# Optimization experiments

Measured on AMD Instinct MI355X. Metric: run time of the kernel, lower is better.

The kernel has to match this reference:

```python
import jax, jax.numpy as jnp
import numpy as np

N, D, H, C, E = 16384, 768, 768, 2, 20

def setup_inputs() -> dict:
    key = jax.random.key(0)
    k1, k2, k3, k4, k5, k6 = jax.random.split(key, 6)
    return {
        "embeddings": jax.random.normal(k1, (N, D), dtype=jnp.float32),
        "component_idx": jax.random.randint(k2, (N,), 0, E, dtype=jnp.int64),
        "W1": jax.random.normal(k3, (E, D, H), dtype=jnp.float32) * (1.0 / np.sqrt(D)),
        "b1": jnp.zeros((E, H), dtype=jnp.float32),
        "W2": jax.random.normal(k4, (E, H, C), dtype=jnp.float32) * (1.0 / np.sqrt(H)),
        "b2": jnp.zeros((E, C), dtype=jnp.float32),
    }

def reference(embeddings, component_idx, W1, b1, W2, b2):
    # Each token n goes through expert component_idx[n]:
    #   y = relu(x @ W1[e] + b1[e]) @ W2[e] + b2[e]
    # The torch module's mask/cat/argsort reassembly is mathematically a
    # per-token select of its own expert's output at the original position.
    # Dense-expert formulation (standard jax MoE fallback), then gather.
    h = jax.nn.relu(jnp.einsum('nd,edh->enh', embeddings, W1) + b1[:, None, :])  # [E,N,H]
    y = jnp.einsum('enh,ehc->enc', h, W2) + b2[:, None, :]                        # [E,N,C]
    n_idx = jnp.arange(embeddings.shape[0])
    return y[component_idx, n_idx]  # [N,C]
```

## Files before the change

kernel.cpp:

```cpp
#include <hip/hip_runtime.h>

#define N_D 768
#define N_H 768
#define N_C 2
#define N_E 20
#define MT 128
#define NT 128
#define BK 32
#define KT (N_D / BK)
#define MAX_TILES 160
#define NCOL (N_H / NT)
#define ROWB (N_D * 2)
#define W1BLKS (N_E * (N_D / 64) * (N_H / 64))
#define SG_TOK 64

typedef __attribute__((ext_vector_type(8))) short short8;
typedef __attribute__((ext_vector_type(4))) float f32x4;

__device__ __forceinline__ unsigned short f2bf(float f) {
  unsigned u = __builtin_bit_cast(unsigned, f);
  u += 0x7FFFu + ((u >> 16) & 1u);
  return (unsigned short)(u >> 16);
}

#define GLD_LDS16(gp, lp)                                                        \
  __builtin_amdgcn_global_load_lds(                                              \
      (const __attribute__((address_space(1))) void*)(gp),                       \
      (__attribute__((address_space(3))) void*)(lp), 16, 0, 0)


__global__ __launch_bounds__(256) void k_front(const int* __restrict__ cidx,
                                               int* __restrict__ counts,
                                               int* __restrict__ offsets,
                                               int* __restrict__ cursor,
                                               int* __restrict__ tiles,
                                               int* __restrict__ numTiles, int n) {
  __shared__ int lc[4][N_E];
  __shared__ int tot[N_E];
  const int tid = threadIdx.x;
  const int w = tid >> 6;
  for (int k = tid; k < 4 * N_E; k += 256) ((int*)lc)[k] = 0;
  __syncthreads();
  const int4* c4 = (const int4*)cidx;
  const int nv = n >> 2;
  for (int i = tid; i < nv; i += 256) {
    int4 v = c4[i];
    int e0 = v.x < 0 ? 0 : (v.x >= N_E ? N_E - 1 : v.x);
    int e1 = v.y < 0 ? 0 : (v.y >= N_E ? N_E - 1 : v.y);
    int e2 = v.z < 0 ? 0 : (v.z >= N_E ? N_E - 1 : v.z);
    int e3 = v.w < 0 ? 0 : (v.w >= N_E ? N_E - 1 : v.w);
    atomicAdd(&lc[w][e0], 1);
    atomicAdd(&lc[w][e1], 1);
    atomicAdd(&lc[w][e2], 1);
    atomicAdd(&lc[w][e3], 1);
  }
  for (int i = (nv << 2) + tid; i < n; i += 256) {
    int e = cidx[i];
    e = e < 0 ? 0 : (e >= N_E ? N_E - 1 : e);
    atomicAdd(&lc[w][e], 1);
  }
  __syncthreads();
  if (tid < N_E) tot[tid] = lc[0][tid] + lc[1][tid] + lc[2][tid] + lc[3][tid];
  __syncthreads();
  if (tid < 64) {
    int lane = tid;
    int c = (lane < N_E) ? tot[lane] : 0;
    int nt = (c + MT - 1) / MT;
    int cs = c, ts = nt;
#pragma unroll
    for (int s = 1; s < 32; s <<= 1) {
      int t1 = __shfl_up(cs, s, 64);
      int t2 = __shfl_up(ts, s, 64);
      if (lane >= s) {
        cs += t1;
        ts += t2;
      }
    }
    int coff = cs - c;
    int tbase = ts - nt;
    if (lane < N_E) {
      counts[lane] = c;
      offsets[lane] = coff;
      cursor[lane] = coff;
      for (int m = 0; m < nt; ++m) {
        int t = tbase + m;
        if (t < MAX_TILES) tiles[t] = (lane << 8) | m;
      }
    }
    if (lane == N_E - 1) *numTiles = ts > MAX_TILES ? MAX_TILES : ts;
  }
}


__global__ __launch_bounds__(256) void k_mid(
    const int* __restrict__ cidx, int* __restrict__ cursor,
    int* __restrict__ sorted, const float* __restrict__ emb,
    unsigned short* __restrict__ Xg, const float* __restrict__ W1,
    unsigned short* __restrict__ W1t, float* __restrict__ out, int n, int nbsg) {
  __shared__ float tile[64][65];
  __shared__ int lc[N_E];
  __shared__ int lbase[N_E];
  __shared__ int pos_s[SG_TOK];
  const int tid = threadIdx.x;

  if ((int)blockIdx.x >= nbsg) {
    int w1i = blockIdx.x - nbsg;
    int xcd = w1i & 7, ii = w1i >> 3;
    int wgid = xcd * (W1BLKS / 8) + ii;
    int e = wgid / 144;
    int rem = wgid - e * 144;
    int h0 = (rem % 12) * 64, d0 = (rem / 12) * 64;
    const float* src = W1 + (size_t)e * N_D * N_H;
    unsigned short* dst = W1t + (size_t)e * N_H * N_D;
    int tx = tid & 15, ty = tid >> 4;
#pragma unroll
    for (int s = 0; s < 4; ++s) {
      int d = s * 16 + ty;
      float4 v = *(const float4*)&src[(size_t)(d0 + d) * N_H + h0 + tx * 4];
      tile[d][tx * 4 + 0] = v.x;
      tile[d][tx * 4 + 1] = v.y;
      tile[d][tx * 4 + 2] = v.z;
      tile[d][tx * 4 + 3] = v.w;
    }
    __syncthreads();
    int px = tid & 7, py = tid >> 3;
#pragma unroll
    for (int s = 0; s < 2; ++s) {
      int h = s * 32 + py;
      short8 v;
#pragma unroll
      for (int j = 0; j < 8; ++j)
        v[j] = (short)f2bf(tile[px * 8 + j][h]);
      *(short8*)&dst[(size_t)(h0 + h) * N_D + d0 + px * 8] = v;
    }
    return;
  }

  const int nb = (n + SG_TOK - 1) / SG_TOK;
  if ((int)blockIdx.x >= nb) {
    ushort4 z = {0, 0, 0, 0};
    ushort4* dst = (ushort4*)(Xg + (size_t)n * N_D);
    for (int k = tid; k < MT * N_D / 4; k += 256) dst[k] = z;
    float4 zf = {0.f, 0.f, 0.f, 0.f};
    float4* of = (float4*)out;
    for (int k = tid; k < N_C * n / 4; k += 256) of[k] = zf;
    return;
  }
  const int base_tok = blockIdx.x * SG_TOK;
  if (tid < N_E) lc[tid] = 0;
  __syncthreads();
  const int i = base_tok + tid;
  int e = 0, p = 0;
  if (tid < SG_TOK && i < n) {
    e = cidx[i];
    e = e < 0 ? 0 : (e >= N_E ? N_E - 1 : e);
    p = atomicAdd(&lc[e], 1);
  }
  __syncthreads();
  if (tid < N_E) lbase[tid] = atomicAdd(&cursor[tid], lc[tid]);
  __syncthreads();
  if (tid < SG_TOK) {
    if (i < n) {
      int pos = lbase[e] + p;
      sorted[pos] = i;
      pos_s[tid] = pos;
    } else {
      pos_s[tid] = -1;
    }
  }
  __syncthreads();
  const int wid = tid >> 6, lane = tid & 63;
  int nrows = n - base_tok;
  if (nrows > SG_TOK) nrows = SG_TOK;
  for (int rr = wid; rr < nrows; rr += 4) {
    const float4* s = (const float4*)(emb + (size_t)(base_tok + rr) * N_D);
    ushort4* d = (ushort4*)(Xg + (size_t)pos_s[rr] * N_D);
#pragma unroll
    for (int p2 = 0; p2 < 3; ++p2) {
      float4 v = s[lane + p2 * 64];
      ushort4 o;
      o.x = f2bf(v.x);
      o.y = f2bf(v.y);
      o.z = f2bf(v.z);
      o.w = f2bf(v.w);
      d[lane + p2 * 64] = o;
    }
  }
}


__global__ __launch_bounds__(256, 2) void k_gemm(
    const unsigned short* __restrict__ Xg, const unsigned short* __restrict__ W1t,
    const float* __restrict__ b1, const float* __restrict__ W2,
    const float* __restrict__ b2, const int* __restrict__ sorted,
    const int* __restrict__ counts, const int* __restrict__ offsets,
    const int* __restrict__ tiles, const int* __restrict__ numTiles,
    float* __restrict__ out) {
  const int nactive = *numTiles * NCOL;
  const int lin = (int)blockIdx.y * NCOL + (int)blockIdx.x;
  if (lin >= nactive) return;
  const int q = nactive >> 3, r = nactive & 7;
  const int c = lin & 7, ii = lin >> 3;
  const int wgid = (c < r ? c * (q + 1) : r * (q + 1) + (c - r) * q) + ii;
  const int tileIdx = wgid / NCOL;
  const int n0 = (wgid - tileIdx * NCOL) * NT;

  const int tv = tiles[tileIdx];
  const int e = tv >> 8;
  const int m0 = (tv & 255) * MT;
  const int off = offsets[e];
  const int cnt_rel = counts[e] - m0;

  __shared__ unsigned short lA[2][MT * BK];
  __shared__ unsigned short lB[2][NT * BK];

  const int tid = threadIdx.x;
  const int wid = tid >> 6, lane = tid & 63;
  const int wm = (wid >> 1) * 64, wn = (wid & 1) * 64;
  const int quad = lane >> 4, lm = lane & 15;

  const int R0 = wid * 32 + lm;
  const char* agp = (const char*)Xg + (size_t)(off + m0 + R0) * ROWB + quad * 16;
  const char* bgp = (const char*)W1t + (size_t)e * N_H * ROWB +
                    (size_t)(n0 + R0) * ROWB + quad * 16;
  unsigned short* lap[2] = {&lA[0][(wid * 32) * BK], &lA[1][(wid * 32) * BK]};
  unsigned short* lbp[2] = {&lB[0][(wid * 32) * BK], &lB[1][(wid * 32) * BK]};

#define ISSUE_BATCH(kk, b)                                                       \
  do {                                                                           \
    const char* a_ = agp + (kk)*64;                                              \
    const char* b_ = bgp + (kk)*64;                                              \
    GLD_LDS16(a_, lap[b]);                                                       \
    GLD_LDS16(a_ + 16 * ROWB, lap[b] + 16 * BK);                                 \
    GLD_LDS16(b_, lbp[b]);                                                       \
    GLD_LDS16(b_ + 16 * ROWB, lbp[b] + 16 * BK);                                 \
  } while (0)

  f32x4 acc[4][4] = {};

  ISSUE_BATCH(0, 0);
  ISSUE_BATCH(1, 1);

  const int fa = quad * 128 + lm * 8;

  for (int kt = 0; kt < KT; ++kt) {
    const int cur = kt & 1;
    asm volatile("s_waitcnt vmcnt(4)\n\ts_barrier" ::: "memory");
    short8 af[4], bfr[4];
    for (int i = 0; i < 4; ++i)
      af[i] = *(const short8*)&lA[cur][((wm >> 4) + i) * 512 + fa];
    for (int j = 0; j < 4; ++j)
      bfr[j] = *(const short8*)&lB[cur][((wn >> 4) + j) * 512 + fa];
    asm volatile("s_waitcnt lgkmcnt(0)\n\ts_barrier" ::: "memory");
    int kk = kt + 2;
    if (kk >= KT) kk -= KT;
    ISSUE_BATCH(kk, cur);
    for (int i = 0; i < 4; ++i)
      for (int j = 0; j < 4; ++j)
        acc[i][j] =
            __builtin_amdgcn_mfma_f32_16x16x32_bf16(af[i], bfr[j], acc[i][j], 0, 0, 0);
  }

  float y0[4][4], y1[4][4];
  for (int i = 0; i < 4; ++i)
    for (int r2 = 0; r2 < 4; ++r2) y0[i][r2] = y1[i][r2] = 0.f;

  for (int j = 0; j < 4; ++j) {
    int col = n0 + wn + j * 16 + lm;
    float bias = b1[e * N_H + col];
    float2 w2 = *(const float2*)&W2[((size_t)e * N_H + col) * N_C];
    for (int i = 0; i < 4; ++i) {
      f32x4 a = acc[i][j];
      for (int r2 = 0; r2 < 4; ++r2) {
        float h = a[r2] + bias;
        h = h > 0.f ? h : 0.f;
        y0[i][r2] += h * w2.x;
        y1[i][r2] += h * w2.y;
      }
    }
  }
  for (int s = 1; s < 16; s <<= 1) {
    for (int i = 0; i < 4; ++i)
      for (int r2 = 0; r2 < 4; ++r2) {
        y0[i][r2] += __shfl_xor(y0[i][r2], s, 64);
        y1[i][r2] += __shfl_xor(y1[i][r2], s, 64);
      }
  }
  if (lm == 0) {
    const bool add_bias = (n0 == 0) && (wn == 0);
    float bb0 = add_bias ? b2[e * N_C + 0] : 0.f;
    float bb1 = add_bias ? b2[e * N_C + 1] : 0.f;
    for (int i = 0; i < 4; ++i) {
      for (int r2 = 0; r2 < 4; ++r2) {
        int mrel = wm + i * 16 + quad * 4 + r2;
        if (mrel < cnt_rel) {
          int token = sorted[off + m0 + mrel];
          atomicAdd(&out[(size_t)token * N_C + 0], y0[i][r2] + bb0);
          atomicAdd(&out[(size_t)token * N_C + 1], y1[i][r2] + bb1);
        }
      }
    }
  }
}


extern "C" void kernel_launch(void* const* d_in, const int* in_sizes, int n_in,
                              void* d_out, int out_size, void* d_ws, size_t ws_size,
                              hipStream_t stream) {
  const float* emb = (const float*)d_in[0];
  const int* cidx = (const int*)d_in[1];
  const float* W1 = (const float*)d_in[2];
  const float* b1 = (const float*)d_in[3];
  const float* W2 = (const float*)d_in[4];
  const float* b2 = (const float*)d_in[5];
  float* out = (float*)d_out;
  const int n = in_sizes[1];

  char* ws = (char*)d_ws;
  int* counts = (int*)ws;
  int* offsets = (int*)(ws + 128);
  int* cursor = (int*)(ws + 256);
  int* numTiles = (int*)(ws + 384);
  int* tiles = (int*)(ws + 512);
  int* sorted = (int*)(ws + 2048);
  size_t sorted_bytes = ((size_t)n * 4 + 255) & ~(size_t)255;
  unsigned short* Xg = (unsigned short*)(ws + 2048 + sorted_bytes);
  int pcap = n + MT;
  unsigned short* W1t = Xg + (size_t)pcap * N_D;

  k_front<<<1, 256, 0, stream>>>(cidx, counts, offsets, cursor, tiles, numTiles, n);
  int nbsg = (n + SG_TOK - 1) / SG_TOK + 1;
  k_mid<<<nbsg + W1BLKS, 256, 0, stream>>>(cidx, cursor, sorted, emb, Xg, W1, W1t,
                                           out, n, nbsg);
  k_gemm<<<dim3(NCOL, MAX_TILES), 256, 0, stream>>>(
      Xg, W1t, b1, W2, b2, sorted, counts, offsets, tiles, numTiles, out);
}
```

Measured before the change: 205.9 us.

## Merge prep kernels and gather token rows inside GEMM instead of pre-scattering

Measured after the change: 212.6 us. 3.3% more time.

```diff
diff --git a/kernel.cpp b/kernel.cpp
--- a/kernel.cpp
+++ b/kernel.cpp
@@ -12,7 +12,7 @@
 #define NCOL (N_H / NT)
 #define ROWB (N_D * 2)
 #define W1BLKS (N_E * (N_D / 64) * (N_H / 64))
-#define SG_TOK 64
+#define XBBLKS 256
 
 typedef __attribute__((ext_vector_type(8))) short short8;
 typedef __attribute__((ext_vector_type(4))) float f32x4;
@@ -29,82 +29,83 @@
       (__attribute__((address_space(3))) void*)(lp), 16, 0, 0)
 
 
-__global__ __launch_bounds__(256) void k_front(const int* __restrict__ cidx,
-                                               int* __restrict__ counts,
-                                               int* __restrict__ offsets,
-                                               int* __restrict__ cursor,
-                                               int* __restrict__ tiles,
-                                               int* __restrict__ numTiles, int n) {
-  __shared__ int lc[4][N_E];
-  __shared__ int tot[N_E];
+__global__ __launch_bounds__(256) void k_prep(
+    const int* __restrict__ cidx, int* __restrict__ counts,
+    int* __restrict__ offsets, int* __restrict__ tiles,
+    int* __restrict__ numTiles, int* __restrict__ sorted,
+    const float* __restrict__ emb, unsigned short* __restrict__ Xb,
+    const float* __restrict__ W1, unsigned short* __restrict__ W1t,
+    float* __restrict__ out, int n) {
   const int tid = threadIdx.x;
-  const int w = tid >> 6;
-  for (int k = tid; k < 4 * N_E; k += 256) ((int*)lc)[k] = 0;
-  __syncthreads();
-  const int4* c4 = (const int4*)cidx;
-  const int nv = n >> 2;
-  for (int i = tid; i < nv; i += 256) {
-    int4 v = c4[i];
-    int e0 = v.x < 0 ? 0 : (v.x >= N_E ? N_E - 1 : v.x);
-    int e1 = v.y < 0 ? 0 : (v.y >= N_E ? N_E - 1 : v.y);
-    int e2 = v.z < 0 ? 0 : (v.z >= N_E ? N_E - 1 : v.z);
-    int e3 = v.w < 0 ? 0 : (v.w >= N_E ? N_E - 1 : v.w);
-    atomicAdd(&lc[w][e0], 1);
-    atomicAdd(&lc[w][e1], 1);
-    atomicAdd(&lc[w][e2], 1);
-    atomicAdd(&lc[w][e3], 1);
-  }
-  for (int i = (nv << 2) + tid; i < n; i += 256) {
-    int e = cidx[i];
-    e = e < 0 ? 0 : (e >= N_E ? N_E - 1 : e);
-    atomicAdd(&lc[w][e], 1);
-  }
-  __syncthreads();
-  if (tid < N_E) tot[tid] = lc[0][tid] + lc[1][tid] + lc[2][tid] + lc[3][tid];
-  __syncthreads();
-  if (tid < 64) {
-    int lane = tid;
-    int c = (lane < N_E) ? tot[lane] : 0;
-    int nt = (c + MT - 1) / MT;
-    int cs = c, ts = nt;
+
+  if (blockIdx.x == 0) {
+    __shared__ int lc[4][N_E];
+    __shared__ int tot[N_E];
+    __shared__ int scur[N_E];
+    const int w = tid >> 6;
+    for (int k = tid; k < 4 * N_E; k += 256) ((int*)lc)[k] = 0;
+    __syncthreads();
+    const int4* c4 = (const int4*)cidx;
+    const int nv = n >> 2;
+    for (int i = tid; i < nv; i += 256) {
+      int4 v = c4[i];
+      int e0 = v.x < 0 ? 0 : (v.x >= N_E ? N_E - 1 : v.x);
+      int e1 = v.y < 0 ? 0 : (v.y >= N_E ? N_E - 1 : v.y);
+      int e2 = v.z < 0 ? 0 : (v.z >= N_E ? N_E - 1 : v.z);
+      int e3 = v.w < 0 ? 0 : (v.w >= N_E ? N_E - 1 : v.w);
+      atomicAdd(&lc[w][e0], 1);
+      atomicAdd(&lc[w][e1], 1);
+      atomicAdd(&lc[w][e2], 1);
+      atomicAdd(&lc[w][e3], 1);
+    }
+    for (int i = (nv << 2) + tid; i < n; i += 256) {
+      int e = cidx[i];
+      e = e < 0 ? 0 : (e >= N_E ? N_E - 1 : e);
+      atomicAdd(&lc[w][e], 1);
+    }
+    __syncthreads();
+    if (tid < N_E) tot[tid] = lc[0][tid] + lc[1][tid] + lc[2][tid] + lc[3][tid];
+    __syncthreads();
+    if (tid < 64) {
+      int lane = tid;
+      int c = (lane < N_E) ? tot[lane] : 0;
+      int nt = (c + MT - 1) / MT;
+      int cs = c, ts = nt;
 #pragma unroll
-    for (int s = 1; s < 32; s <<= 1) {
-      int t1 = __shfl_up(cs, s, 64);
-      int t2 = __shfl_up(ts, s, 64);
-      if (lane >= s) {
-        cs += t1;
-        ts += t2;
-      }
-    }
-    int coff = cs - c;
-    int tbase = ts - nt;
-    if (lane < N_E) {
-      counts[lane] = c;
-      offsets[lane] = coff;
-      cursor[lane] = coff;
-      for (int m = 0; m < nt; ++m) {
-        int t = tbase + m;
-        if (t < MAX_TILES) tiles[t] = (lane << 8) | m;
-      }
-    }
-    if (lane == N_E - 1) *numTiles = ts > MAX_TILES ? MAX_TILES : ts;
-  }
-}
-
-
-__global__ __launch_bounds__(256) void k_mid(
-    const int* __restrict__ cidx, int* __restrict__ cursor,
-    int* __restrict__ sorted, const float* __restrict__ emb,
-    unsigned short* __restrict__ Xg, const float* __restrict__ W1,
-    unsigned short* __restrict__ W1t, float* __restrict__ out, int n, int nbsg) {
-  __shared__ float tile[64][65];
-  __shared__ int lc[N_E];
-  __shared__ int lbase[N_E];
-  __shared__ int pos_s[SG_TOK];
-  const int tid = threadIdx.x;
-
-  if ((int)blockIdx.x >= nbsg) {
-    int w1i = blockIdx.x - nbsg;
+      for (int s = 1; s < 32; s <<= 1) {
+        int t1 = __shfl_up(cs, s, 64);
+        int t2 = __shfl_up(ts, s, 64);
+        if (lane >= s) {
+          cs += t1;
+          ts += t2;
+        }
+      }
+      int coff = cs - c;
+      int tbase = ts - nt;
+      if (lane < N_E) {
+        counts[lane] = c;
+        offsets[lane] = coff;
+        scur[lane] = coff;
+        for (int m = 0; m < nt; ++m) {
+          int t = tbase + m;
+          if (t < MAX_TILES) tiles[t] = (lane << 8) | m;
+        }
+      }
+      if (lane == N_E - 1) *numTiles = ts > MAX_TILES ? MAX_TILES : ts;
+    }
+    __syncthreads();
+    for (int i = tid; i < n; i += 256) {
+      int e = cidx[i];
+      e = e < 0 ? 0 : (e >= N_E ? N_E - 1 : e);
+      int p = atomicAdd(&scur[e], 1);
+      sorted[p] = i;
+    }
+    return;
+  }
+
+  if ((int)blockIdx.x < 1 + W1BLKS) {
+    __shared__ float tile[64][65];
+    int w1i = blockIdx.x - 1;
     int xcd = w1i & 7, ii = w1i >> 3;
     int wgid = xcd * (W1BLKS / 8) + ii;
     int e = wgid / 144;
@@ -136,66 +137,34 @@
     return;
   }
 
-  const int nb = (n + SG_TOK - 1) / SG_TOK;
-  if ((int)blockIdx.x >= nb) {
-    ushort4 z = {0, 0, 0, 0};
-    ushort4* dst = (ushort4*)(Xg + (size_t)n * N_D);
-    for (int k = tid; k < MT * N_D / 4; k += 256) dst[k] = z;
+  int xb = blockIdx.x - 1 - W1BLKS;
+  const float4* s4 = (const float4*)emb;
+  ushort4* d4 = (ushort4*)Xb;
+  const int total = n * (N_D / 4);
+  for (int k = xb * 256 + tid; k < total; k += XBBLKS * 256) {
+    float4 v = s4[k];
+    ushort4 o;
+    o.x = f2bf(v.x);
+    o.y = f2bf(v.y);
+    o.z = f2bf(v.z);
+    o.w = f2bf(v.w);
+    d4[k] = o;
+  }
+  if (xb < 8) {
     float4 zf = {0.f, 0.f, 0.f, 0.f};
     float4* of = (float4*)out;
-    for (int k = tid; k < N_C * n / 4; k += 256) of[k] = zf;
-    return;
-  }
-  const int base_tok = blockIdx.x * SG_TOK;
-  if (tid < N_E) lc[tid] = 0;
-  __syncthreads();
-  const int i = base_tok + tid;
-  int e = 0, p = 0;
-  if (tid < SG_TOK && i < n) {
-    e = cidx[i];
-    e = e < 0 ? 0 : (e >= N_E ? N_E - 1 : e);
-    p = atomicAdd(&lc[e], 1);
-  }
-  __syncthreads();
-  if (tid < N_E) lbase[tid] = atomicAdd(&cursor[tid], lc[tid]);
-  __syncthreads();
-  if (tid < SG_TOK) {
-    if (i < n) {
-      int pos = lbase[e] + p;
-      sorted[pos] = i;
-      pos_s[tid] = pos;
-    } else {
-      pos_s[tid] = -1;
-    }
-  }
-  __syncthreads();
-  const int wid = tid >> 6, lane = tid & 63;
-  int nrows = n - base_tok;
-  if (nrows > SG_TOK) nrows = SG_TOK;
-  for (int rr = wid; rr < nrows; rr += 4) {
-    const float4* s = (const float4*)(emb + (size_t)(base_tok + rr) * N_D);
-    ushort4* d = (ushort4*)(Xg + (size_t)pos_s[rr] * N_D);
-#pragma unroll
-    for (int p2 = 0; p2 < 3; ++p2) {
-      float4 v = s[lane + p2 * 64];
-      ushort4 o;
-      o.x = f2bf(v.x);
-      o.y = f2bf(v.y);
-      o.z = f2bf(v.z);
-      o.w = f2bf(v.w);
-      d[lane + p2 * 64] = o;
-    }
+    for (int k = xb * 256 + tid; k < n * N_C / 4; k += 8 * 256) of[k] = zf;
   }
 }
 
 
 __global__ __launch_bounds__(256, 2) void k_gemm(
-    const unsigned short* __restrict__ Xg, const unsigned short* __restrict__ W1t,
+    const unsigned short* __restrict__ Xb, const unsigned short* __restrict__ W1t,
     const float* __restrict__ b1, const float* __restrict__ W2,
     const float* __restrict__ b2, const int* __restrict__ sorted,
     const int* __restrict__ counts, const int* __restrict__ offsets,
     const int* __restrict__ tiles, const int* __restrict__ numTiles,
-    float* __restrict__ out) {
+    float* __restrict__ out, int n) {
   const int nactive = *numTiles * NCOL;
   const int lin = (int)blockIdx.y * NCOL + (int)blockIdx.x;
   if (lin >= nactive) return;
@@ -220,7 +189,12 @@
   const int quad = lane >> 4, lm = lane & 15;
 
   const int R0 = wid * 32 + lm;
-  const char* agp = (const char*)Xg + (size_t)(off + m0 + R0) * ROWB + quad * 16;
+  const int pos0 = off + m0 + R0;
+  const int pos1 = pos0 + 16;
+  const int t0 = sorted[pos0 < n ? pos0 : 0];
+  const int t1 = sorted[pos1 < n ? pos1 : 0];
+  const char* agp0 = (const char*)Xb + (size_t)t0 * ROWB + quad * 16;
+  const char* agp1 = (const char*)Xb + (size_t)t1 * ROWB + quad * 16;
   const char* bgp = (const char*)W1t + (size_t)e * N_H * ROWB +
                     (size_t)(n0 + R0) * ROWB + quad * 16;
   unsigned short* lap[2] = {&lA[0][(wid * 32) * BK], &lA[1][(wid * 32) * BK]};
@@ -228,10 +202,9 @@
 
 #define ISSUE_BATCH(kk, b)                                                       \
   do {                                                                           \
-    const char* a_ = agp + (kk)*64;                                              \
     const char* b_ = bgp + (kk)*64;                                              \
-    GLD_LDS16(a_, lap[b]);                                                       \
-    GLD_LDS16(a_ + 16 * ROWB, lap[b] + 16 * BK);                                 \
+    GLD_LDS16(agp0 + (kk)*64, lap[b]);                                           \
+    GLD_LDS16(agp1 + (kk)*64, lap[b] + 16 * BK);                                 \
     GLD_LDS16(b_, lbp[b]);                                                       \
     GLD_LDS16(b_ + 16 * ROWB, lbp[b] + 16 * BK);                                 \
   } while (0)
@@ -319,19 +292,15 @@
   char* ws = (char*)d_ws;
   int* counts = (int*)ws;
   int* offsets = (int*)(ws + 128);
-  int* cursor = (int*)(ws + 256);
   int* numTiles = (int*)(ws + 384);
   int* tiles = (int*)(ws + 512);
   int* sorted = (int*)(ws + 2048);
   size_t sorted_bytes = ((size_t)n * 4 + 255) & ~(size_t)255;
-  unsigned short* Xg = (unsigned short*)(ws + 2048 + sorted_bytes);
-  int pcap = n + MT;
-  unsigned short* W1t = Xg + (size_t)pcap * N_D;
-
-  k_front<<<1, 256, 0, stream>>>(cidx, counts, offsets, cursor, tiles, numTiles, n);
-  int nbsg = (n + SG_TOK - 1) / SG_TOK + 1;
-  k_mid<<<nbsg + W1BLKS, 256, 0, stream>>>(cidx, cursor, sorted, emb, Xg, W1, W1t,
-                                           out, n, nbsg);
+  unsigned short* Xb = (unsigned short*)(ws + 2048 + sorted_bytes);
+  unsigned short* W1t = Xb + (size_t)n * N_D;
+
+  k_prep<<<1 + W1BLKS + XBBLKS, 256, 0, stream>>>(
+      cidx, counts, offsets, tiles, numTiles, sorted, emb, Xb, W1, W1t, out, n);
   k_gemm<<<dim3(NCOL, MAX_TILES), 256, 0, stream>>>(
-      Xg, W1t, b1, W2, b2, sorted, counts, offsets, tiles, numTiles, out);
+      Xb, W1t, b1, W2, b2, sorted, counts, offsets, tiles, numTiles, out, n);
 }
```

## Halve GEMM M-tile to 64 with triple-buffered LDS and higher occupancy

Applied to the files above, without the earlier changes.

Result: slower. 220.5 us (+7.1%).

```diff
diff --git a/kernel.cpp b/kernel.cpp
--- a/kernel.cpp
+++ b/kernel.cpp
@@ -5,10 +5,11 @@
 #define N_C 2
 #define N_E 20
 #define MT 128
+#define MTA 64
 #define NT 128
 #define BK 32
 #define KT (N_D / BK)
-#define MAX_TILES 160
+#define MAX_TILES 288
 #define NCOL (N_H / NT)
 #define ROWB (N_D * 2)
 #define W1BLKS (N_E * (N_D / 64) * (N_H / 64))
@@ -65,7 +66,7 @@
   if (tid < 64) {
     int lane = tid;
     int c = (lane < N_E) ? tot[lane] : 0;
-    int nt = (c + MT - 1) / MT;
+    int nt = (c + MTA - 1) / MTA;
     int cs = c, ts = nt;
 #pragma unroll
     for (int s = 1; s < 32; s <<= 1) {
@@ -84,7 +85,7 @@
       cursor[lane] = coff;
       for (int m = 0; m < nt; ++m) {
         int t = tbase + m;
-        if (t < MAX_TILES) tiles[t] = (lane << 8) | m;
+        if (t < MAX_TILES) tiles[t] = (lane << 10) | m;
       }
     }
     if (lane == N_E - 1) *numTiles = ts > MAX_TILES ? MAX_TILES : ts;
@@ -189,7 +190,7 @@
 }
 
 
-__global__ __launch_bounds__(256, 2) void k_gemm(
+__global__ __launch_bounds__(256, 4) void k_gemm(
     const unsigned short* __restrict__ Xg, const unsigned short* __restrict__ W1t,
     const float* __restrict__ b1, const float* __restrict__ W2,
     const float* __restrict__ b2, const int* __restrict__ sorted,
@@ -206,70 +207,70 @@
   const int n0 = (wgid - tileIdx * NCOL) * NT;
 
   const int tv = tiles[tileIdx];
-  const int e = tv >> 8;
-  const int m0 = (tv & 255) * MT;
+  const int e = tv >> 10;
+  const int m0 = (tv & 1023) * MTA;
   const int off = offsets[e];
   const int cnt_rel = counts[e] - m0;
 
-  __shared__ unsigned short lA[2][MT * BK];
-  __shared__ unsigned short lB[2][NT * BK];
+  __shared__ unsigned short lA[3][MTA * BK];
+  __shared__ unsigned short lB[3][NT * BK];
 
   const int tid = threadIdx.x;
   const int wid = tid >> 6, lane = tid & 63;
-  const int wm = (wid >> 1) * 64, wn = (wid & 1) * 64;
+  const int wr = wid >> 1, wc = wid & 1;
   const int quad = lane >> 4, lm = lane & 15;
 
-  const int R0 = wid * 32 + lm;
-  const char* agp = (const char*)Xg + (size_t)(off + m0 + R0) * ROWB + quad * 16;
+  const char* agp =
+      (const char*)Xg + (size_t)(off + m0 + wid * 16 + lm) * ROWB + quad * 16;
   const char* bgp = (const char*)W1t + (size_t)e * N_H * ROWB +
-                    (size_t)(n0 + R0) * ROWB + quad * 16;
-  unsigned short* lap[2] = {&lA[0][(wid * 32) * BK], &lA[1][(wid * 32) * BK]};
-  unsigned short* lbp[2] = {&lB[0][(wid * 32) * BK], &lB[1][(wid * 32) * BK]};
+                    (size_t)(n0 + wid * 32 + lm) * ROWB + quad * 16;
 
 #define ISSUE_BATCH(kk, b)                                                       \
   do {                                                                           \
-    const char* a_ = agp + (kk)*64;                                              \
-    const char* b_ = bgp + (kk)*64;                                              \
-    GLD_LDS16(a_, lap[b]);                                                       \
-    GLD_LDS16(a_ + 16 * ROWB, lap[b] + 16 * BK);                                 \
-    GLD_LDS16(b_, lbp[b]);                                                       \
-    GLD_LDS16(b_ + 16 * ROWB, lbp[b] + 16 * BK);                                 \
+    GLD_LDS16(agp + (kk)*64, &lA[b][wid * 512]);                                 \
+    GLD_LDS16(bgp + (kk)*64, &lB[b][wid * 1024]);                                \
+    GLD_LDS16(bgp + 16 * ROWB + (kk)*64, &lB[b][wid * 1024 + 512]);              \
   } while (0)
 
-  f32x4 acc[4][4] = {};
+  f32x4 acc[2][4] = {};
 
   ISSUE_BATCH(0, 0);
   ISSUE_BATCH(1, 1);
+  ISSUE_BATCH(2, 2);
 
   const int fa = quad * 128 + lm * 8;
 
   for (int kt = 0; kt < KT; ++kt) {
-    const int cur = kt & 1;
-    asm volatile("s_waitcnt vmcnt(4)\n\ts_barrier" ::: "memory");
-    short8 af[4], bfr[4];
-    for (int i = 0; i < 4; ++i)
-      af[i] = *(const short8*)&lA[cur][((wm >> 4) + i) * 512 + fa];
+    const int cur = kt % 3;
+    asm volatile("s_waitcnt vmcnt(6)\n\ts_barrier" ::: "memory");
+    short8 af[2], bfr[4];
+#pragma unroll
+    for (int i = 0; i < 2; ++i)
+      af[i] = *(const short8*)&lA[cur][(wr * 2 + i) * 512 + fa];
+#pragma unroll
     for (int j = 0; j < 4; ++j)
-      bfr[j] = *(const short8*)&lB[cur][((wn >> 4) + j) * 512 + fa];
+      bfr[j] = *(const short8*)&lB[cur][(wc * 4 + j) * 512 + fa];
     asm volatile("s_waitcnt lgkmcnt(0)\n\ts_barrier" ::: "memory");
-    int kk = kt + 2;
+    int kk = kt + 3;
     if (kk >= KT) kk -= KT;
     ISSUE_BATCH(kk, cur);
-    for (int i = 0; i < 4; ++i)
+#pragma unroll
+    for (int i = 0; i < 2; ++i)
+#pragma unroll
       for (int j = 0; j < 4; ++j)
         acc[i][j] =
             __builtin_amdgcn_mfma_f32_16x16x32_bf16(af[i], bfr[j], acc[i][j], 0, 0, 0);
   }
 
-  float y0[4][4], y1[4][4];
-  for (int i = 0; i < 4; ++i)
+  float y0[2][4], y1[2][4];
+  for (int i = 0; i < 2; ++i)
     for (int r2 = 0; r2 < 4; ++r2) y0[i][r2] = y1[i][r2] = 0.f;
 
   for (int j = 0; j < 4; ++j) {
-    int col = n0 + wn + j * 16 + lm;
+    int col = n0 + wc * 64 + j * 16 + lm;
     float bias = b1[e * N_H + col];
     float2 w2 = *(const float2*)&W2[((size_t)e * N_H + col) * N_C];
-    for (int i = 0; i < 4; ++i) {
+    for (int i = 0; i < 2; ++i) {
       f32x4 a = acc[i][j];
       for (int r2 = 0; r2 < 4; ++r2) {
         float h = a[r2] + bias;
@@ -280,19 +281,19 @@
     }
   }
   for (int s = 1; s < 16; s <<= 1) {
-    for (int i = 0; i < 4; ++i)
+    for (int i = 0; i < 2; ++i)
       for (int r2 = 0; r2 < 4; ++r2) {
         y0[i][r2] += __shfl_xor(y0[i][r2], s, 64);
         y1[i][r2] += __shfl_xor(y1[i][r2], s, 64);
       }
   }
   if (lm == 0) {
-    const bool add_bias = (n0 == 0) && (wn == 0);
+    const bool add_bias = (n0 == 0) && (wc == 0);
     float bb0 = add_bias ? b2[e * N_C + 0] : 0.f;
     float bb1 = add_bias ? b2[e * N_C + 1] : 0.f;
-    for (int i = 0; i < 4; ++i) {
+    for (int i = 0; i < 2; ++i) {
       for (int r2 = 0; r2 < 4; ++r2) {
-        int mrel = wm + i * 16 + quad * 4 + r2;
+        int mrel = wr * 32 + i * 16 + quad * 4 + r2;
         if (mrel < cnt_rel) {
           int token = sorted[off + m0 + mrel];
           atomicAdd(&out[(size_t)token * N_C + 0], y0[i][r2] + bb0);
```
